# Kernel optimization log

Hardware: AMD Instinct MI355X
Metric: run time of the kernel (lower is better)

Reference implementation:

```python
import jax, jax.numpy as jnp
import numpy as np

# DAG: node -> list of children; node 0 is the stem output, node 6 is the cell output.
GRAPH = {1: [0], 2: [0, 1], 3: [1, 2], 4: [2, 3], 5: [3, 4], 6: [4, 5]}
OUTPUT_NODE = 6


def conv3x3(x, w, b):
    # x: [N,C,H,W], w: [O,I,3,3], b: [O]; stride 1, SAME padding (PyTorch Conv2d pad=1)
    y = jax.lax.conv_general_dilated(
        x, w, window_strides=(1, 1), padding='SAME',
        dimension_numbers=('NCHW', 'OIHW', 'NCHW'))
    return y + b[None, :, None, None]


def setup_inputs() -> dict:
    key = jax.random.key(0)
    k_x, k_w0, k_b0, k_wn, k_bn = jax.random.split(key, 5)
    scale = 0.05  # keep activations bounded through 7 stacked convs
    return {
        'x': jax.random.normal(k_x, (8, 64, 64, 64), dtype=jnp.float32),
        'W0': jax.random.normal(k_w0, (128, 64, 3, 3), dtype=jnp.float32) * scale,
        'b0': jax.random.normal(k_b0, (128,), dtype=jnp.float32) * scale,
        'Wn': jax.random.normal(k_wn, (6, 128, 128, 3, 3), dtype=jnp.float32) * scale,
        'bn': jax.random.normal(k_bn, (6, 128), dtype=jnp.float32) * scale,
    }


def reference(x, W0, b0, Wn, bn):
    # activations[0] = layers['0'](x)
    acts = {0: conv3x3(x, W0, b0)}
    # DFS with memoization over a DAG == topological evaluation of nodes 1..6.
    # Each node n sums its OWN conv (weights Wn[n-1]) applied to every child activation.
    for node in range(1, OUTPUT_NODE + 1):
        w, b = Wn[node - 1], bn[node - 1]
        out = None
        for child in GRAPH[node]:
            y = conv3x3(acts[child], w, b)
            out = y if out is None else out + y
        acts[node] = out
    return acts[OUTPUT_NODE]
```

## Files before the change

kernel.cpp:

```cpp
#include <hip/hip_runtime.h>


typedef __bf16 bf16x8 __attribute__((ext_vector_type(8)));
typedef float f32x4 __attribute__((ext_vector_type(4)));

union U4 { uint4 u; bf16x8 b; };

__device__ inline unsigned pk_bf16(float lo, float hi) {
  unsigned r;
  asm volatile("v_cvt_pk_bf16_f32 %0, %1, %2" : "=v"(r) : "v"(lo), "v"(hi));
  return r;
}

__device__ inline unsigned addpk(unsigned a, unsigned b) {
  float alo = __builtin_bit_cast(float, a << 16);
  float ahi = __builtin_bit_cast(float, a & 0xFFFF0000u);
  float blo = __builtin_bit_cast(float, b << 16);
  float bhi = __builtin_bit_cast(float, b & 0xFFFF0000u);
  return pk_bf16(alo + blo, ahi + bhi);
}

__device__ inline uint4 addpk4(uint4 a, uint4 b) {
  return make_uint4(addpk(a.x, b.x), addpk(a.y, b.y), addpk(a.z, b.z), addpk(a.w, b.w));
}

#define WB_WORDS 479232

__global__ __launch_bounds__(512) void setup_all(
    const float* __restrict__ x, const float* __restrict__ W0,
    const float* __restrict__ Wn, unsigned* __restrict__ B0,
    unsigned* __restrict__ B1, unsigned* __restrict__ B2,
    unsigned* __restrict__ T, unsigned* __restrict__ Wb) {
  __shared__ float xl[2 * 64 * 65];
  const int tid = threadIdx.x;
  const int bid = blockIdx.x;
  const int n = bid & 7;

#pragma unroll
  for (int it = 0; it < 4; ++it) {
    unsigned gid = (unsigned)bid * 512 + tid + it * 131072u;
    if (gid < WB_WORDS) {
      const float* src;
      int CIN, c, w;
      if (gid < 36864) {
        src = W0; CIN = 64;
        c = gid >> 11; w = gid & 2047;
      } else {
        unsigned g2 = gid - 36864;
        int s = g2 / 73728; unsigned r2 = g2 % 73728;
        src = Wn + (size_t)s * 147456; CIN = 128;
        c = r2 >> 12; w = r2 & 4095;
      }
      int och = c / 9, tap = c % 9;
      int dy = tap / 3, dx = tap % 3;
      int f = w >> 8;
      int nkc = CIN / 32;
      int m = f / nkc, kc = f % nkc;
      int r8 = w & 255;
      int lane = r8 >> 2, wq = r8 & 3;
      int oc = och * 64 + m * 16 + (lane & 15);
      int icp = kc * 16 + (lane >> 4) * 4 + wq;
      size_t base = (((size_t)oc * CIN + 2 * icp) * 3 + dy) * 3 + dx;
      Wb[gid] = pk_bf16(src[base], src[base + 9]);
    }
  }

  {
    unsigned gid = (unsigned)bid * 512 + tid;
    if (gid < 116480) {
      unsigned* buf; int CW; unsigned u;
      if (gid < 99840) {
        buf = gid < 33280 ? B0 : (gid < 66560 ? B1 : B2);
        u = gid % 33280; CW = 64;
      } else {
        buf = T; u = gid - 99840; CW = 32;
      }
      int per_n = 65 * CW;
      int nn = u / per_n;
      unsigned v = u % per_n;
      int pix = (v * 4) / CW, cw = (v * 4) % CW;
      int row, col;
      if (pix < 66) { row = 0; col = pix; }
      else if (pix < 132) { row = 65; col = pix - 66; }
      else if (pix < 196) { row = pix - 131; col = 0; }
      else { row = pix - 195; col = 65; }
      *(uint4*)&buf[((((size_t)nn * 66 + row) * 66 + col) * CW) + cw] =
          make_uint4(0, 0, 0, 0);
    }
  }

  {
    int hh = bid >> 3;
    int sub = tid >> 8;
    int t8 = tid & 255;
    int h = hh * 2 + sub;
#pragma unroll
    for (int k = 0; k < 16; ++k) {
      int idx = t8 + k * 256;
      int ic = idx >> 6, w = idx & 63;
      xl[(sub * 64 + w) * 65 + ic] = x[(((size_t)n * 64 + ic) * 64 + h) * 64 + w];
    }
    __syncthreads();
#pragma unroll
    for (int k = 0; k < 8; ++k) {
      int idx = t8 + k * 256;
      int w = idx >> 5, icp = idx & 31;
      unsigned v = pk_bf16(xl[(sub * 64 + w) * 65 + icp * 2],
                           xl[(sub * 64 + w) * 65 + icp * 2 + 1]);
      int wp = w + 1;
      int pos = icp ^ ((wp & 7) << 2);
      T[(((size_t)n * 66 + (h + 1)) * 66 + wp) * 32 + pos] = v;
    }
  }
}

template <int CIN, bool DUAL, bool OUTF32>
__global__ __launch_bounds__(512, 2) void conv_stage(
    const unsigned* __restrict__ in0, const unsigned* __restrict__ in1,
    const unsigned* __restrict__ wb, const float* __restrict__ bias,
    float bmult, void* __restrict__ outp) {
  constexpr int WPP = CIN / 2;
  constexpr int CHW = 64 * WPP;
  constexpr int CH_U4 = CHW / 4;
  constexpr int NKC_TOT = WPP / 16;
  constexpr int KCW = NKC_TOT / 2;
  constexpr int ROWW = 66 * WPP;
  constexpr int ACTW = 6 * ROWW;
  constexpr int ALDS_W = (ACTW > 16384) ? ACTW : 16384;
  constexpr int R4_U4 = 4 * ROWW / 4;
  constexpr int R2_U4 = 2 * ROWW / 4;
  constexpr int AJ4 = (R4_U4 + 511) / 512;
  constexpr int LJ = (R2_U4 + 511) / 512;

  __shared__ unsigned Alds[ALDS_W];

  const int tid = threadIdx.x;
  const int lane = tid & 63;
  const int wav = tid >> 6;
  const int wr = wav >> 1;
  const int kh = wav & 1;
  const int l15 = lane & 15, q = lane >> 4;
  const int bid = blockIdx.x;
  const int n = bid & 7;
  const int ochalf = (bid >> 3) & 1;
  const int h0 = (bid >> 4) * 4;

  const uint4* wg = (const uint4*)(wb + (size_t)ochalf * 9 * CHW);
  const size_t abase = ((size_t)n * 66 + h0) * ROWW;
  const uint4* g0 = (const uint4*)(in0 + abase);
  const uint4* g1 = (const uint4*)(in1 + abase);

#pragma unroll
  for (int j = 0; j < AJ4; ++j) {
    int i = tid + j * 512;
    if (i < R4_U4) {
      uint4 v = g0[i];
      if (DUAL) v = addpk4(v, g1[i]);
      *(uint4*)&Alds[4 * i] = v;
    }
  }

  uint4 wcur[4][KCW], wnxt[4][KCW];
#pragma unroll
  for (int m = 0; m < 4; ++m)
#pragma unroll
    for (int kc2 = 0; kc2 < KCW; ++kc2)
      wcur[m][kc2] = wg[(m * NKC_TOT + kh * KCW + kc2) * 64 + lane];

  __syncthreads();

  f32x4 acc[4][4];
#pragma unroll
  for (int m = 0; m < 4; ++m)
#pragma unroll
    for (int p = 0; p < 4; ++p) acc[m][p] = (f32x4)0.f;

#pragma unroll
  for (int t = 0; t < 9; ++t) {
    if (t == 3) {
      asm volatile("s_waitcnt lgkmcnt(0)" ::: "memory");
      __builtin_amdgcn_s_barrier();
      __builtin_amdgcn_sched_barrier(0);
    }

    if (t < 8) {
#pragma unroll
      for (int m = 0; m < 4; ++m)
#pragma unroll
        for (int kc2 = 0; kc2 < KCW; ++kc2)
          wnxt[m][kc2] =
              wg[(t + 1) * CH_U4 + (m * NKC_TOT + kh * KCW + kc2) * 64 + lane];
    }

    const int dy = t / 3, dx = t % 3;
    const int arow = (wr + dy) * 66;

    __builtin_amdgcn_s_setprio(1);
#pragma unroll
    for (int kc2 = 0; kc2 < KCW; ++kc2) {
      const int kc = kh * KCW + kc2;
      bf16x8 a[4];
#pragma unroll
      for (int m = 0; m < 4; ++m) {
        U4 u; u.u = wcur[m][kc2]; a[m] = u.b;
      }
#pragma unroll
      for (int p = 0; p < 4; ++p) {
        int col = p * 16 + l15 + dx;
        U4 u;
        u.u = *(const uint4*)&Alds[(arow + col) * WPP +
                                   ((kc * 16 + q * 4) ^ ((col & 7) << 2))];
        bf16x8 b = u.b;
#pragma unroll
        for (int m = 0; m < 4; ++m)
          acc[m][p] =
              __builtin_amdgcn_mfma_f32_16x16x32_bf16(a[m], b, acc[m][p], 0, 0, 0);
      }
    }
    __builtin_amdgcn_s_setprio(0);

    if (t == 0) {
#pragma unroll
      for (int j = 0; j < LJ; ++j) {
        int i = tid + j * 512;
        if (i < R2_U4) {
          uint4 v = g0[R4_U4 + i];
          if (DUAL) v = addpk4(v, g1[R4_U4 + i]);
          *(uint4*)&Alds[4 * (R4_U4 + i)] = v;
        }
      }
    }

#pragma unroll
    for (int m = 0; m < 4; ++m)
#pragma unroll
      for (int kc2 = 0; kc2 < KCW; ++kc2) wcur[m][kc2] = wnxt[m][kc2];
  }

  __syncthreads();
  float* R = (float*)Alds;
  if (kh) {
#pragma unroll
    for (int m = 0; m < 4; ++m) {
      *(f32x4*)&R[(((wr * 2 + 1) * 8) + m * 2 + 0) * 256 + lane * 4] = acc[m][0];
      *(f32x4*)&R[(((wr * 2 + 1) * 8) + m * 2 + 1) * 256 + lane * 4] = acc[m][1];
    }
  } else {
#pragma unroll
    for (int m = 0; m < 4; ++m) {
      *(f32x4*)&R[(((wr * 2 + 0) * 8) + m * 2 + 0) * 256 + lane * 4] = acc[m][2];
      *(f32x4*)&R[(((wr * 2 + 0) * 8) + m * 2 + 1) * 256 + lane * 4] = acc[m][3];
    }
  }
  __syncthreads();
  if (kh) {
#pragma unroll
    for (int m = 0; m < 4; ++m) {
      acc[m][2] += *(const f32x4*)&R[(((wr * 2 + 0) * 8) + m * 2 + 0) * 256 + lane * 4];
      acc[m][3] += *(const f32x4*)&R[(((wr * 2 + 0) * 8) + m * 2 + 1) * 256 + lane * 4];
    }
  } else {
#pragma unroll
    for (int m = 0; m < 4; ++m) {
      acc[m][0] += *(const f32x4*)&R[(((wr * 2 + 1) * 8) + m * 2 + 0) * 256 + lane * 4];
      acc[m][1] += *(const f32x4*)&R[(((wr * 2 + 1) * 8) + m * 2 + 1) * 256 + lane * 4];
    }
  }

  const int obase = ochalf * 64;
#define EPI_F32(P)                                                              \
  {                                                                             \
    _Pragma("unroll") for (int m = 0; m < 4; ++m) {                             \
      int oc0 = obase + m * 16 + q * 4;                                         \
      float4 bb = *(const float4*)&bias[oc0];                                   \
      int w = (P) * 16 + l15;                                                   \
      _Pragma("unroll") for (int j = 0; j < 4; ++j)                             \
          ((float*)outp)[(((size_t)n * 128 + oc0 + j) * 64 + (h0 + wr)) * 64 +  \
                         w] = acc[m][(P)][j] + ((const float*)&bb)[j] * bmult;  \
    }                                                                           \
  }
#define EPI_BF16(P)                                                             \
  {                                                                             \
    _Pragma("unroll") for (int m = 0; m < 4; ++m) {                             \
      int oc0 = obase + m * 16 + q * 4;                                         \
      float4 bb = *(const float4*)&bias[oc0];                                   \
      int icp0 = oc0 >> 1;                                                      \
      int w = (P) * 16 + l15;                                                   \
      int wp = w + 1;                                                           \
      unsigned lo = pk_bf16(acc[m][(P)][0] + bb.x * bmult,                      \
                            acc[m][(P)][1] + bb.y * bmult);                     \
      unsigned hi = pk_bf16(acc[m][(P)][2] + bb.z * bmult,                      \
                            acc[m][(P)][3] + bb.w * bmult);                     \
      int pos = icp0 ^ ((wp & 7) << 2);                                         \
      size_t base = (((size_t)n * 66 + (h0 + 1 + wr)) * 66 + wp) * 64;          \
      *(uint2*)&((unsigned*)outp)[base + pos] = make_uint2(lo, hi);             \
    }                                                                           \
  }
  if (OUTF32) {
    if (kh) { EPI_F32(2); EPI_F32(3); }
    else    { EPI_F32(0); EPI_F32(1); }
  } else {
    if (kh) { EPI_BF16(2); EPI_BF16(3); }
    else    { EPI_BF16(0); EPI_BF16(1); }
  }
#undef EPI_F32
#undef EPI_BF16
}

extern "C" void kernel_launch(void* const* d_in, const int* in_sizes, int n_in,
                              void* d_out, int out_size, void* d_ws,
                              size_t ws_size, hipStream_t stream) {
  const float* x = (const float*)d_in[0];
  const float* W0 = (const float*)d_in[1];
  const float* b0 = (const float*)d_in[2];
  const float* Wn = (const float*)d_in[3];
  const float* bn = (const float*)d_in[4];

  const size_t ACTB = (size_t)8 * 66 * 66 * 64;
  const size_t TW = (size_t)8 * 66 * 66 * 32;
  unsigned* B0 = (unsigned*)d_ws;
  unsigned* B1 = B0 + ACTB;
  unsigned* B2 = B1 + ACTB;
  unsigned* T = B2 + ACTB;
  unsigned* Wb = T + TW;

  setup_all<<<256, 512, 0, stream>>>(x, W0, Wn, B0, B1, B2, T, Wb);

  dim3 grid(256), blk(512);
  const unsigned* Wnode = Wb + 36864;
  const size_t NW = 73728;

  conv_stage<64, false, false><<<grid, blk, 0, stream>>>(T, T, Wb, b0, 1.f, B0);
  conv_stage<128, false, false><<<grid, blk, 0, stream>>>(B0, B0, Wnode, bn + 0, 1.f, B1);
  conv_stage<128, true, false><<<grid, blk, 0, stream>>>(B0, B1, Wnode + 1 * NW, bn + 128, 2.f, B2);
  conv_stage<128, true, false><<<grid, blk, 0, stream>>>(B1, B2, Wnode + 2 * NW, bn + 256, 2.f, B0);
  conv_stage<128, true, false><<<grid, blk, 0, stream>>>(B2, B0, Wnode + 3 * NW, bn + 384, 2.f, B1);
  conv_stage<128, true, false><<<grid, blk, 0, stream>>>(B0, B1, Wnode + 4 * NW, bn + 512, 2.f, B2);
  conv_stage<128, true, true><<<grid, blk, 0, stream>>>(B1, B2, Wnode + 5 * NW, bn + 640, 2.f, d_out);

  (void)in_sizes; (void)n_in; (void)out_size; (void)ws_size;
}
```

Before: 106.8 us.

## Switch conv MFMA tiles from 16x16x32 to 32x32x16 bf16

Replaces the 16x16x32 bf16 MFMA with the 32x32x16 variant, so each wave computes 2x2 tiles of 32x32 instead of 4x4 tiles of 16x16. The weight pre-pack layout, the LDS operand addressing, the split-K reduction through LDS and the epilogues are all rewritten to match the 32x32 accumulator layout. The goal is fewer LDS B-operand reads per MFMA and better operand reuse per instruction. The cost is a more complex epilogue and reduction mapping and a different register footprint.

```diff
diff --git a/kernel.cpp b/kernel.cpp
--- a/kernel.cpp
+++ b/kernel.cpp
@@ -3,6 +3,7 @@
 
 typedef __bf16 bf16x8 __attribute__((ext_vector_type(8)));
 typedef float f32x4 __attribute__((ext_vector_type(4)));
+typedef float f32x16 __attribute__((ext_vector_type(16)));
 
 union U4 { uint4 u; bf16x8 b; };
 
@@ -53,13 +54,15 @@
       }
       int och = c / 9, tap = c % 9;
       int dy = tap / 3, dx = tap % 3;
+      int NKS = CIN / 32;
       int f = w >> 8;
-      int nkc = CIN / 32;
-      int m = f / nkc, kc = f % nkc;
+      int m = f / (2 * NKS);
+      int rem = f % (2 * NKS);
+      int kh = rem / NKS, ks = rem % NKS;
       int r8 = w & 255;
       int lane = r8 >> 2, wq = r8 & 3;
-      int oc = och * 64 + m * 16 + (lane & 15);
-      int icp = kc * 16 + (lane >> 4) * 4 + wq;
+      int oc = och * 64 + m * 32 + (lane & 31);
+      int icp = kh * (CIN / 4) + ks * 8 + (lane >> 5) * 4 + wq;
       size_t base = (((size_t)oc * CIN + 2 * icp) * 3 + dy) * 3 + dx;
       Wb[gid] = pk_bf16(src[base], src[base + 9]);
     }
@@ -122,8 +125,7 @@
   constexpr int WPP = CIN / 2;
   constexpr int CHW = 64 * WPP;
   constexpr int CH_U4 = CHW / 4;
-  constexpr int NKC_TOT = WPP / 16;
-  constexpr int KCW = NKC_TOT / 2;
+  constexpr int NKS = CIN / 32;
   constexpr int ROWW = 66 * WPP;
   constexpr int ACTW = 6 * ROWW;
   constexpr int ALDS_W = (ACTW > 16384) ? ACTW : 16384;
@@ -139,7 +141,7 @@
   const int wav = tid >> 6;
   const int wr = wav >> 1;
   const int kh = wav & 1;
-  const int l15 = lane & 15, q = lane >> 4;
+  const int l31 = lane & 31, h32 = lane >> 5;
   const int bid = blockIdx.x;
   const int n = bid & 7;
   const int ochalf = (bid >> 3) & 1;
@@ -160,20 +162,20 @@
     }
   }
 
-  uint4 wcur[4][KCW], wnxt[4][KCW];
-#pragma unroll
-  for (int m = 0; m < 4; ++m)
-#pragma unroll
-    for (int kc2 = 0; kc2 < KCW; ++kc2)
-      wcur[m][kc2] = wg[(m * NKC_TOT + kh * KCW + kc2) * 64 + lane];
+  uint4 wcur[2][NKS], wnxt[2][NKS];
+#pragma unroll
+  for (int m = 0; m < 2; ++m)
+#pragma unroll
+    for (int ks = 0; ks < NKS; ++ks)
+      wcur[m][ks] = wg[((m * 2 + kh) * NKS + ks) * 64 + lane];
 
   __syncthreads();
 
-  f32x4 acc[4][4];
-#pragma unroll
-  for (int m = 0; m < 4; ++m)
-#pragma unroll
-    for (int p = 0; p < 4; ++p) acc[m][p] = (f32x4)0.f;
+  f32x16 acc[2][2];
+#pragma unroll
+  for (int m = 0; m < 2; ++m)
+#pragma unroll
+    for (int p = 0; p < 2; ++p) acc[m][p] = (f32x16)0.f;
 
 #pragma unroll
   for (int t = 0; t < 9; ++t) {
@@ -185,11 +187,11 @@
 
     if (t < 8) {
 #pragma unroll
-      for (int m = 0; m < 4; ++m)
-#pragma unroll
-        for (int kc2 = 0; kc2 < KCW; ++kc2)
-          wnxt[m][kc2] =
-              wg[(t + 1) * CH_U4 + (m * NKC_TOT + kh * KCW + kc2) * 64 + lane];
+      for (int m = 0; m < 2; ++m)
+#pragma unroll
+        for (int ks = 0; ks < NKS; ++ks)
+          wnxt[m][ks] =
+              wg[(t + 1) * CH_U4 + ((m * 2 + kh) * NKS + ks) * 64 + lane];
     }
 
     const int dy = t / 3, dx = t % 3;
@@ -197,24 +199,19 @@
 
     __builtin_amdgcn_s_setprio(1);
 #pragma unroll
-    for (int kc2 = 0; kc2 < KCW; ++kc2) {
-      const int kc = kh * KCW + kc2;
-      bf16x8 a[4];
-#pragma unroll
-      for (int m = 0; m < 4; ++m) {
-        U4 u; u.u = wcur[m][kc2]; a[m] = u.b;
-      }
-#pragma unroll
-      for (int p = 0; p < 4; ++p) {
-        int col = p * 16 + l15 + dx;
+    for (int ks = 0; ks < NKS; ++ks) {
+      bf16x8 a0, a1;
+      { U4 u; u.u = wcur[0][ks]; a0 = u.b; }
+      { U4 u; u.u = wcur[1][ks]; a1 = u.b; }
+      const int wb0 = kh * (WPP / 2) + ks * 8 + h32 * 4;
+#pragma unroll
+      for (int p = 0; p < 2; ++p) {
+        int col = p * 32 + l31 + dx;
         U4 u;
-        u.u = *(const uint4*)&Alds[(arow + col) * WPP +
-                                   ((kc * 16 + q * 4) ^ ((col & 7) << 2))];
+        u.u = *(const uint4*)&Alds[(arow + col) * WPP + (wb0 ^ ((col & 7) << 2))];
         bf16x8 b = u.b;
-#pragma unroll
-        for (int m = 0; m < 4; ++m)
-          acc[m][p] =
-              __builtin_amdgcn_mfma_f32_16x16x32_bf16(a[m], b, acc[m][p], 0, 0, 0);
+        acc[0][p] = __builtin_amdgcn_mfma_f32_32x32x16_bf16(a0, b, acc[0][p], 0, 0, 0);
+        acc[1][p] = __builtin_amdgcn_mfma_f32_32x32x16_bf16(a1, b, acc[1][p], 0, 0, 0);
       }
     }
     __builtin_amdgcn_s_setprio(0);
@@ -232,76 +229,97 @@
     }
 
 #pragma unroll
-    for (int m = 0; m < 4; ++m)
-#pragma unroll
-      for (int kc2 = 0; kc2 < KCW; ++kc2) wcur[m][kc2] = wnxt[m][kc2];
+    for (int m = 0; m < 2; ++m)
+#pragma unroll
+      for (int ks = 0; ks < NKS; ++ks) wcur[m][ks] = wnxt[m][ks];
   }
 
   __syncthreads();
   float* R = (float*)Alds;
   if (kh) {
 #pragma unroll
-    for (int m = 0; m < 4; ++m) {
-      *(f32x4*)&R[(((wr * 2 + 1) * 8) + m * 2 + 0) * 256 + lane * 4] = acc[m][0];
-      *(f32x4*)&R[(((wr * 2 + 1) * 8) + m * 2 + 1) * 256 + lane * 4] = acc[m][1];
-    }
+    for (int m = 0; m < 2; ++m)
+#pragma unroll
+      for (int qt = 0; qt < 4; ++qt) {
+        f32x4 tv;
+        tv[0] = acc[m][0][4 * qt + 0]; tv[1] = acc[m][0][4 * qt + 1];
+        tv[2] = acc[m][0][4 * qt + 2]; tv[3] = acc[m][0][4 * qt + 3];
+        *(f32x4*)&R[((((wr * 2 + 1) * 2 + m) * 4) + qt) * 256 + lane * 4] = tv;
+      }
   } else {
 #pragma unroll
-    for (int m = 0; m < 4; ++m) {
-      *(f32x4*)&R[(((wr * 2 + 0) * 8) + m * 2 + 0) * 256 + lane * 4] = acc[m][2];
-      *(f32x4*)&R[(((wr * 2 + 0) * 8) + m * 2 + 1) * 256 + lane * 4] = acc[m][3];
-    }
+    for (int m = 0; m < 2; ++m)
+#pragma unroll
+      for (int qt = 0; qt < 4; ++qt) {
+        f32x4 tv;
+        tv[0] = acc[m][1][4 * qt + 0]; tv[1] = acc[m][1][4 * qt + 1];
+        tv[2] = acc[m][1][4 * qt + 2]; tv[3] = acc[m][1][4 * qt + 3];
+        *(f32x4*)&R[((((wr * 2 + 0) * 2 + m) * 4) + qt) * 256 + lane * 4] = tv;
+      }
   }
   __syncthreads();
   if (kh) {
 #pragma unroll
-    for (int m = 0; m < 4; ++m) {
-      acc[m][2] += *(const f32x4*)&R[(((wr * 2 + 0) * 8) + m * 2 + 0) * 256 + lane * 4];
-      acc[m][3] += *(const f32x4*)&R[(((wr * 2 + 0) * 8) + m * 2 + 1) * 256 + lane * 4];
-    }
+    for (int m = 0; m < 2; ++m)
+#pragma unroll
+      for (int qt = 0; qt < 4; ++qt) {
+        f32x4 o = *(const f32x4*)&R[((((wr * 2 + 0) * 2 + m) * 4) + qt) * 256 + lane * 4];
+        acc[m][1][4 * qt + 0] += o[0]; acc[m][1][4 * qt + 1] += o[1];
+        acc[m][1][4 * qt + 2] += o[2]; acc[m][1][4 * qt + 3] += o[3];
+      }
   } else {
 #pragma unroll
-    for (int m = 0; m < 4; ++m) {
-      acc[m][0] += *(const f32x4*)&R[(((wr * 2 + 1) * 8) + m * 2 + 0) * 256 + lane * 4];
-      acc[m][1] += *(const f32x4*)&R[(((wr * 2 + 1) * 8) + m * 2 + 1) * 256 + lane * 4];
-    }
+    for (int m = 0; m < 2; ++m)
+#pragma unroll
+      for (int qt = 0; qt < 4; ++qt) {
+        f32x4 o = *(const f32x4*)&R[((((wr * 2 + 1) * 2 + m) * 4) + qt) * 256 + lane * 4];
+        acc[m][0][4 * qt + 0] += o[0]; acc[m][0][4 * qt + 1] += o[1];
+        acc[m][0][4 * qt + 2] += o[2]; acc[m][0][4 * qt + 3] += o[3];
+      }
   }
 
   const int obase = ochalf * 64;
 #define EPI_F32(P)                                                              \
   {                                                                             \
-    _Pragma("unroll") for (int m = 0; m < 4; ++m) {                             \
-      int oc0 = obase + m * 16 + q * 4;                                         \
-      float4 bb = *(const float4*)&bias[oc0];                                   \
-      int w = (P) * 16 + l15;                                                   \
-      _Pragma("unroll") for (int j = 0; j < 4; ++j)                             \
-          ((float*)outp)[(((size_t)n * 128 + oc0 + j) * 64 + (h0 + wr)) * 64 +  \
-                         w] = acc[m][(P)][j] + ((const float*)&bb)[j] * bmult;  \
+    _Pragma("unroll") for (int m = 0; m < 2; ++m) {                             \
+      int ocb = obase + m * 32;                                                 \
+      int w = (P) * 32 + l31;                                                   \
+      _Pragma("unroll") for (int g = 0; g < 4; ++g) {                           \
+        int oc4 = ocb + 8 * g + 4 * h32;                                        \
+        float4 bb = *(const float4*)&bias[oc4];                                 \
+        _Pragma("unroll") for (int s = 0; s < 4; ++s)                           \
+            ((float*)outp)[(((size_t)n * 128 + oc4 + s) * 64 + (h0 + wr)) * 64 +\
+                           w] = acc[m][(P)][4 * g + s] +                        \
+                                ((const float*)&bb)[s] * bmult;                 \
+      }                                                                         \
     }                                                                           \
   }
 #define EPI_BF16(P)                                                             \
   {                                                                             \
-    _Pragma("unroll") for (int m = 0; m < 4; ++m) {                             \
-      int oc0 = obase + m * 16 + q * 4;                                         \
-      float4 bb = *(const float4*)&bias[oc0];                                   \
-      int icp0 = oc0 >> 1;                                                      \
-      int w = (P) * 16 + l15;                                                   \
+    _Pragma("unroll") for (int m = 0; m < 2; ++m) {                             \
+      int ocb = obase + m * 32;                                                 \
+      int icpb = ocb >> 1;                                                      \
+      int w = (P) * 32 + l31;                                                   \
       int wp = w + 1;                                                           \
-      unsigned lo = pk_bf16(acc[m][(P)][0] + bb.x * bmult,                      \
-                            acc[m][(P)][1] + bb.y * bmult);                     \
-      unsigned hi = pk_bf16(acc[m][(P)][2] + bb.z * bmult,                      \
-                            acc[m][(P)][3] + bb.w * bmult);                     \
-      int pos = icp0 ^ ((wp & 7) << 2);                                         \
-      size_t base = (((size_t)n * 66 + (h0 + 1 + wr)) * 66 + wp) * 64;          \
-      *(uint2*)&((unsigned*)outp)[base + pos] = make_uint2(lo, hi);             \
+      int xorv = (wp & 7) << 2;                                                 \
+      size_t gb = (((size_t)n * 66 + (h0 + 1 + wr)) * 66 + wp) * 64;            \
+      _Pragma("unroll") for (int g = 0; g < 4; ++g) {                           \
+        int oc4 = ocb + 8 * g + 4 * h32;                                        \
+        float4 bb = *(const float4*)&bias[oc4];                                 \
+        float v0 = acc[m][(P)][4 * g + 0] + bb.x * bmult;                       \
+        float v1 = acc[m][(P)][4 * g + 1] + bb.y * bmult;                       \
+        float v2 = acc[m][(P)][4 * g + 2] + bb.z * bmult;                       \
+        float v3 = acc[m][(P)][4 * g + 3] + bb.w * bmult;                       \
+        int pos = (icpb + 4 * g + 2 * h32) ^ xorv;                              \
+        *(uint2*)&((unsigned*)outp)[gb + pos] =                                 \
+            make_uint2(pk_bf16(v0, v1), pk_bf16(v2, v3));                       \
+      }                                                                         \
     }                                                                           \
   }
   if (OUTF32) {
-    if (kh) { EPI_F32(2); EPI_F32(3); }
-    else    { EPI_F32(0); EPI_F32(1); }
+    if (kh) EPI_F32(1) else EPI_F32(0)
   } else {
-    if (kh) { EPI_BF16(2); EPI_BF16(3); }
-    else    { EPI_BF16(0); EPI_BF16(1); }
+    if (kh) EPI_BF16(1) else EPI_BF16(0)
   }
 #undef EPI_F32
 #undef EPI_BF16
```

Result: slower. 113.6 us (+6.4%).
